# Kernel tuning notes

Measured on AMD Instinct MI355X. Metric: run time of the kernel, lower is better.

The kernel has to match this reference:

```python
import jax, jax.numpy as jnp
import numpy as np

B, D, L, N, M, K = 256, 512, 196, 1024, 512, 10000  # batch, context, num_ctx, hidden, embed, vocab


def setup_inputs() -> dict:
    key = jax.random.key(0)
    ks = jax.random.split(key, 20)
    r = lambda k, s: jax.random.normal(k, s, dtype=jnp.float32) * 0.02
    return {
        "a_i": jax.random.normal(ks[0], (B, D, L), dtype=jnp.float32),
        "inp": jax.random.normal(ks[1], (B, 1, K), dtype=jnp.float32),
        "hn_prev": jax.random.normal(ks[2], (B, 1, N), dtype=jnp.float32),
        "cn_prev": jax.random.normal(ks[3], (B, 1, N), dtype=jnp.float32),
        "f_att_w": r(ks[4], (N + D,)),  # Linear(n+D -> 1), stored as a vector
        "f_att_b": r(ks[5], (1,)),
        "gate_w": r(ks[6], (N,)),       # Linear(n -> 1)
        "gate_b": r(ks[7], (1,)),
        "E_w": r(ks[8], (M, K)),        # torch Linear weight [out, in]
        "E_b": r(ks[9], (M,)),
        "W_ih": r(ks[10], (4 * N, D + N + M)),  # LSTM input->hidden (i,f,g,o)
        "W_hh": r(ks[11], (4 * N, N)),
        "b_ih": r(ks[12], (4 * N,)),
        "b_hh": r(ks[13], (4 * N,)),
        "Lh_w": r(ks[14], (M, N)),
        "Lh_b": r(ks[15], (M,)),
        "Lz_w": r(ks[16], (M, D)),
        "Lz_b": r(ks[17], (M,)),
        "Lo_w": r(ks[18], (K, M)),
        "Lo_b": r(ks[19], (K,)),
    }


def reference(a_i, inp, hn_prev, cn_prev,
              f_att_w, f_att_b, gate_w, gate_b,
              E_w, E_b, W_ih, W_hh, b_ih, b_hh,
              Lh_w, Lh_b, Lz_w, Lz_b, Lo_w, Lo_b):
    h = hn_prev[:, 0]  # [B, N]
    c = cn_prev[:, 0]  # [B, N]
    # --- additive attention: the 196-iteration torch loop batched into one einsum ---
    # cat((a_i[:,:,i], h)) @ f_att_w splits into the a-part and h-part of the weight.
    w_a, w_h = f_att_w[:D], f_att_w[D:]
    e = jnp.einsum('bdl,d->bl', a_i, w_a) + (h @ w_h)[:, None] + f_att_b  # [B, L]
    alpha = jax.nn.softmax(e, axis=1)                                     # [B, L]
    beta = jax.nn.sigmoid(h @ gate_w + gate_b)                            # [B]
    z = beta[:, None] * jnp.einsum('bl,bdl->bd', alpha, a_i)              # [B, D]
    # --- word embedding ---
    w_emb = inp[:, 0] @ E_w.T + E_b                                       # [B, M]
    # --- single-step LSTM (PyTorch gate order i, f, g, o) ---
    x = jnp.concatenate([w_emb, h, z], axis=1)                            # [B, M+N+D]
    gates = x @ W_ih.T + b_ih + h @ W_hh.T + b_hh                         # [B, 4N]
    i_g, f_g, g_g, o_g = jnp.split(gates, 4, axis=1)
    cn = jax.nn.sigmoid(f_g) * c + jax.nn.sigmoid(i_g) * jnp.tanh(g_g)
    hn = jax.nn.sigmoid(o_g) * jnp.tanh(cn)
    # --- output projection ---
    deep_out = w_emb + (hn @ Lh_w.T + Lh_b) + (z @ Lz_w.T + Lz_b)         # [B, M]
    p_yt = deep_out @ Lo_w.T + Lo_b                                       # [B, K]
    return (p_yt[:, None, :], hn[:, None, :], cn[:, None, :], alpha[:, None, :])
```

## Files before the change

kernel.cpp:

```cpp
#include <hip/hip_runtime.h>
#include <hip/hip_bf16.h>
#include <math.h>

#define BB 256
#define DD 512
#define LL 196
#define NN 1024
#define MM 512
#define KK 10000

#define OUT_PY 0
#define OUT_HN ((size_t)2560000)
#define OUT_CN ((size_t)2822144)
#define OUT_AL ((size_t)3084288)

typedef __attribute__((ext_vector_type(8))) short short8v;
typedef __attribute__((ext_vector_type(4))) float f32x4;

__device__ __forceinline__ unsigned short f2bf(float f) {
    unsigned int u = __builtin_bit_cast(unsigned int, f);
    u += 0x7fffu + ((u >> 16) & 1u);
    return (unsigned short)(u >> 16);
}

__device__ __forceinline__ short8v stage8(const float* __restrict__ p, bool ok,
                                          int kbase, int Ktot) {
    short8v v;
    if (ok && (kbase + 7 < Ktot)) {
        const float4 x = *(const float4*)(p + kbase);
        const float4 y = *(const float4*)(p + kbase + 4);
        v[0] = (short)f2bf(x.x); v[1] = (short)f2bf(x.y);
        v[2] = (short)f2bf(x.z); v[3] = (short)f2bf(x.w);
        v[4] = (short)f2bf(y.x); v[5] = (short)f2bf(y.y);
        v[6] = (short)f2bf(y.z); v[7] = (short)f2bf(y.w);
    } else {
#pragma unroll
        for (int i = 0; i < 8; ++i) {
            const int k = kbase + i;
            const float f = (ok && k < Ktot) ? p[k] : 0.f;
            v[i] = (short)f2bf(f);
        }
    }
    return v;
}

__global__ __launch_bounds__(256) void att_e_partial(
    const float* __restrict__ a_i, const float* __restrict__ f_att_w,
    float* __restrict__ pe)
{
    const int b = blockIdx.x, ch = blockIdx.y;
    const int l = threadIdx.x;
    if (l >= LL) return;
    const float* ap = a_i + ((size_t)b * DD + ch * 64) * LL + l;
    const float* wp = f_att_w + ch * 64;
    float s = 0.f;
#pragma unroll 16
    for (int d = 0; d < 64; ++d) s += ap[(size_t)d * LL] * wp[d];
    pe[((size_t)b * 8 + ch) * LL + l] = s;
}

__global__ __launch_bounds__(256) void att_softmax(
    const float* __restrict__ pe, const float* __restrict__ h,
    const float* __restrict__ f_att_w, const float* __restrict__ f_att_b,
    const float* __restrict__ gate_w, const float* __restrict__ gate_b,
    float* __restrict__ alpha_out, float* __restrict__ beta)
{
    const int b = blockIdx.x;
    const int t = threadIdx.x;
    __shared__ float red[256];
    __shared__ float red2[256];

    const float4 h4 = *(const float4*)(h + (size_t)b * NN + t * 4);
    const float4 w4 = *(const float4*)(f_att_w + DD + t * 4);
    const float4 g4 = *(const float4*)(gate_w + t * 4);
    float hd = h4.x * w4.x + h4.y * w4.y + h4.z * w4.z + h4.w * w4.w;
    float gd = h4.x * g4.x + h4.y * g4.y + h4.z * g4.z + h4.w * g4.w;
    red[t] = hd; red2[t] = gd;
    __syncthreads();
    for (int s = 128; s > 0; s >>= 1) {
        if (t < s) { red[t] += red[t + s]; red2[t] += red2[t + s]; }
        __syncthreads();
    }
    const float hdot = red[0];
    const float gdot = red2[0];
    __syncthreads();

    float e = -3.4e38f;
    if (t < LL) {
        const float* p = pe + (size_t)b * 8 * LL + t;
        e = hdot + f_att_b[0];
#pragma unroll
        for (int ch = 0; ch < 8; ++ch) e += p[ch * LL];
    }
    red[t] = e;
    __syncthreads();
    for (int s = 128; s > 0; s >>= 1) {
        if (t < s) red[t] = fmaxf(red[t], red[t + s]);
        __syncthreads();
    }
    const float mx = red[0];
    __syncthreads();
    const float ex = (t < LL) ? expf(e - mx) : 0.f;
    red[t] = ex;
    __syncthreads();
    for (int s = 128; s > 0; s >>= 1) {
        if (t < s) red[t] += red[t + s];
        __syncthreads();
    }
    const float inv = 1.f / red[0];
    if (t < LL) alpha_out[(size_t)b * LL + t] = ex * inv;
    if (t == 0) beta[b] = 1.f / (1.f + expf(-(gdot + gate_b[0])));
}

__global__ __launch_bounds__(256) void att_z(
    const float* __restrict__ a_i, const float* __restrict__ alpha,
    const float* __restrict__ beta, float* __restrict__ z)
{
    const int b = blockIdx.x;
    const int wave = threadIdx.x >> 6, lane = threadIdx.x & 63;
    const int d = blockIdx.y * 4 + wave;
    const float* ap = a_i + ((size_t)b * DD + d) * LL;
    const float* alp = alpha + (size_t)b * LL;
    float s = 0.f;
#pragma unroll
    for (int i = 0; i < 4; ++i) {
        const int l = lane + i * 64;
        if (l < LL) s += ap[l] * alp[l];
    }
#pragma unroll
    for (int off = 32; off > 0; off >>= 1) s += __shfl_down(s, off, 64);
    if (lane == 0) z[(size_t)b * DD + d] = beta[b] * s;
}

__global__ __launch_bounds__(256) void gemm_tn_dual(
    const float* __restrict__ A1, int lda1, const float* __restrict__ B1, int ldb1,
    int kt1n, int K1,
    const float* __restrict__ A2, int lda2, const float* __restrict__ B2, int ldb2,
    int kt2n, int K2,
    float* __restrict__ C, int ldc, int Ncols, int ktPerSplit,
    const float* __restrict__ bias)
{
    __shared__ __align__(16) short As[2][64][72];
    __shared__ __align__(16) short Bs[2][64][72];
    const int t = threadIdx.x;
    const int row0 = blockIdx.x * 64;
    const int col0 = blockIdx.y * 64;
    const int ktTot = kt1n + kt2n;
    const int kt0 = blockIdx.z * ktPerSplit;
    const int nk = min(ktTot, kt0 + ktPerSplit) - kt0;

    const int sr = t >> 2;
    const int sk = (t & 3) << 4;
    const int bc = col0 + sr;
    const bool bok = (bc < Ncols);
    const float* aP1 = A1 + (size_t)(row0 + sr) * lda1;
    const float* bP1 = B1 + (size_t)(bok ? bc : 0) * ldb1;
    const float* aP2 = A2 ? (A2 + (size_t)(row0 + sr) * lda2) : aP1;
    const float* bP2 = A2 ? (B2 + (size_t)(bok ? bc : 0) * ldb2) : bP1;

    const int l = t & 63, w = t >> 6;
    const int wrow = (w >> 1) * 32, wcol = (w & 1) * 32;
    const int lr = l & 15, g = l >> 4, g8 = g * 8;

    f32x4 acc[2][2] = {};

    short8v sa0, sa1, sb0, sb1;
    {
        const int ktg = kt0;
        const float* aR; const float* bR; int kk, Kt;
        if (ktg < kt1n) { aR = aP1; bR = bP1; kk = (ktg << 6) + sk; Kt = K1; }
        else            { aR = aP2; bR = bP2; kk = ((ktg - kt1n) << 6) + sk; Kt = K2; }
        sa0 = stage8(aR, true, kk, Kt);  sa1 = stage8(aR, true, kk + 8, Kt);
        sb0 = stage8(bR, bok,  kk, Kt);  sb1 = stage8(bR, bok,  kk + 8, Kt);
    }
    *(short8v*)&As[0][sr][sk] = sa0; *(short8v*)&As[0][sr][sk + 8] = sa1;
    *(short8v*)&Bs[0][sr][sk] = sb0; *(short8v*)&Bs[0][sr][sk + 8] = sb1;
    __syncthreads();

    int cur = 0;
    for (int kt = 0; kt < nk; ++kt) {
        const bool more = (kt + 1 < nk);
        if (more) {
            const int ktg = kt0 + kt + 1;
            const float* aR; const float* bR; int kk, Kt;
            if (ktg < kt1n) { aR = aP1; bR = bP1; kk = (ktg << 6) + sk; Kt = K1; }
            else            { aR = aP2; bR = bP2; kk = ((ktg - kt1n) << 6) + sk; Kt = K2; }
            sa0 = stage8(aR, true, kk, Kt);  sa1 = stage8(aR, true, kk + 8, Kt);
            sb0 = stage8(bR, bok,  kk, Kt);  sb1 = stage8(bR, bok,  kk + 8, Kt);
        }
#pragma unroll
        for (int ks = 0; ks < 2; ++ks) {
            const int ko = ks * 32 + g8;
            short8v a0 = *(const short8v*)&As[cur][wrow + lr][ko];
            short8v a1 = *(const short8v*)&As[cur][wrow + 16 + lr][ko];
            short8v b0 = *(const short8v*)&Bs[cur][wcol + lr][ko];
            short8v b1 = *(const short8v*)&Bs[cur][wcol + 16 + lr][ko];
            acc[0][0] = __builtin_amdgcn_mfma_f32_16x16x32_bf16(a0, b0, acc[0][0], 0, 0, 0);
            acc[0][1] = __builtin_amdgcn_mfma_f32_16x16x32_bf16(a0, b1, acc[0][1], 0, 0, 0);
            acc[1][0] = __builtin_amdgcn_mfma_f32_16x16x32_bf16(a1, b0, acc[1][0], 0, 0, 0);
            acc[1][1] = __builtin_amdgcn_mfma_f32_16x16x32_bf16(a1, b1, acc[1][1], 0, 0, 0);
        }
        if (more) {
            *(short8v*)&As[cur ^ 1][sr][sk] = sa0;
            *(short8v*)&As[cur ^ 1][sr][sk + 8] = sa1;
            *(short8v*)&Bs[cur ^ 1][sr][sk] = sb0;
            *(short8v*)&Bs[cur ^ 1][sr][sk + 8] = sb1;
        }
        __syncthreads();
        cur ^= 1;
    }

    float* Cp = C + (size_t)blockIdx.z * ((size_t)gridDim.x * 64) * ldc;
#pragma unroll
    for (int m = 0; m < 2; ++m)
#pragma unroll
        for (int n = 0; n < 2; ++n)
#pragma unroll
            for (int j = 0; j < 4; ++j) {
                const int r = row0 + wrow + m * 16 + g * 4 + j;
                const int c = col0 + wcol + n * 16 + lr;
                if (c < Ncols) {
                    float v = acc[m][n][j];
                    if (bias) v += bias[c];
                    Cp[(size_t)r * ldc + c] = v;
                }
            }
}

__global__ __launch_bounds__(256) void build_x(
    const float* __restrict__ embp, int nEmb, const float* __restrict__ E_b,
    const float* __restrict__ h, const float* __restrict__ z,
    float* __restrict__ x)
{
    const int idx = blockIdx.x * 256 + threadIdx.x;
    const int b = idx >> 11, j = idx & 2047;
    float v;
    if (j < 512) {
        v = E_b[j];
        for (int s = 0; s < nEmb; ++s) v += embp[(size_t)s * BB * 512 + (size_t)b * 512 + j];
    } else if (j < 1536) {
        v = h[(size_t)b * NN + (j - 512)];
    } else {
        v = z[(size_t)b * DD + (j - 1536)];
    }
    x[idx] = v;
}

__global__ __launch_bounds__(256) void lstm_cell(
    const float* __restrict__ gatesp, int nG,
    const float* __restrict__ b_ih, const float* __restrict__ b_hh,
    const float* __restrict__ c_prev, float* __restrict__ hn, float* __restrict__ cn)
{
    const int idx = blockIdx.x * 256 + threadIdx.x;
    const int b = idx >> 10, n = idx & 1023;
    float g[4];
#pragma unroll
    for (int gi = 0; gi < 4; ++gi) {
        const int col = gi * 1024 + n;
        const size_t o = (size_t)b * 4096 + col;
        float v = b_ih[col] + b_hh[col];
        for (int s = 0; s < nG; ++s) v += gatesp[(size_t)s * BB * 4096 + o];
        g[gi] = v;
    }
    const float si = 1.f / (1.f + expf(-g[0]));
    const float sf = 1.f / (1.f + expf(-g[1]));
    const float so = 1.f / (1.f + expf(-g[3]));
    const float tg = tanhf(g[2]);
    const float c = c_prev[idx];
    const float cnv = sf * c + si * tg;
    const float hnv = so * tanhf(cnv);
    cn[idx] = cnv;
    hn[idx] = hnv;
}

__global__ __launch_bounds__(256) void build_deep(
    const float* __restrict__ x, const float* __restrict__ dp, int nD,
    const float* __restrict__ Lh_b, const float* __restrict__ Lz_b,
    float* __restrict__ deep)
{
    const int idx = blockIdx.x * 256 + threadIdx.x;
    const int b = idx >> 9, j = idx & 511;
    float v = x[(size_t)b * 2048 + j] + Lh_b[j] + Lz_b[j];
    for (int s = 0; s < nD; ++s) v += dp[(size_t)s * BB * 512 + idx];
    deep[idx] = v;
}

extern "C" void kernel_launch(void* const* d_in, const int* in_sizes, int n_in,
                              void* d_out, int out_size, void* d_ws, size_t ws_size,
                              hipStream_t stream)
{
    const float* a_i     = (const float*)d_in[0];
    const float* inp     = (const float*)d_in[1];
    const float* hn_prev = (const float*)d_in[2];
    const float* cn_prev = (const float*)d_in[3];
    const float* f_att_w = (const float*)d_in[4];
    const float* f_att_b = (const float*)d_in[5];
    const float* gate_w  = (const float*)d_in[6];
    const float* gate_b  = (const float*)d_in[7];
    const float* E_w     = (const float*)d_in[8];
    const float* E_b     = (const float*)d_in[9];
    const float* W_ih    = (const float*)d_in[10];
    const float* W_hh    = (const float*)d_in[11];
    const float* b_ih    = (const float*)d_in[12];
    const float* b_hh    = (const float*)d_in[13];
    const float* Lh_w    = (const float*)d_in[14];
    const float* Lh_b    = (const float*)d_in[15];
    const float* Lz_w    = (const float*)d_in[16];
    const float* Lz_b    = (const float*)d_in[17];
    const float* Lo_w    = (const float*)d_in[18];
    const float* Lo_b    = (const float*)d_in[19];

    float* out = (float*)d_out;
    float* ws  = (float*)d_ws;

    const size_t off_pe   = 0;
    const size_t off_beta = 401408;
    const size_t off_z    = 401664;
    const size_t off_x    = 532736;
    const size_t off_deep = 1057024;
    const size_t small_end = 1188096;

    const size_t avail = ws_size / sizeof(float);
    const bool big = (avail >= small_end + (size_t)4194304);
    const int embS = big ? 16 : 4;
    const int gS   = big ? 4 : 2;
    const int dS   = big ? 12 : 4;
    const size_t off_r1 = small_end;

    float* EMBP   = ws + off_r1;
    float* GATESP = ws + off_r1;
    float* DP     = ws + off_r1;

    att_e_partial<<<dim3(BB, 8), 256, 0, stream>>>(a_i, f_att_w, ws + off_pe);
    att_softmax<<<BB, 256, 0, stream>>>(ws + off_pe, hn_prev, f_att_w, f_att_b,
                                        gate_w, gate_b, out + OUT_AL, ws + off_beta);
    att_z<<<dim3(BB, DD / 4), 256, 0, stream>>>(a_i, out + OUT_AL, ws + off_beta,
                                                ws + off_z);

    gemm_tn_dual<<<dim3(4, 8, embS), 256, 0, stream>>>(
        inp, KK, E_w, KK, 157, KK,
        nullptr, 0, nullptr, 0, 0, 0,
        EMBP, MM, MM, (157 + embS - 1) / embS, nullptr);

    build_x<<<BB * 2048 / 256, 256, 0, stream>>>(EMBP, embS, E_b, hn_prev,
                                                 ws + off_z, ws + off_x);

    gemm_tn_dual<<<dim3(4, 64, gS), 256, 0, stream>>>(
        ws + off_x, 2048, W_ih, 2048, 32, 2048,
        hn_prev, NN, W_hh, NN, 16, NN,
        GATESP, 4096, 4096, 48 / gS, nullptr);

    lstm_cell<<<BB * NN / 256, 256, 0, stream>>>(GATESP, gS, b_ih, b_hh,
                                                 cn_prev, out + OUT_HN, out + OUT_CN);

    gemm_tn_dual<<<dim3(4, 8, dS), 256, 0, stream>>>(
        out + OUT_HN, NN, Lh_w, NN, 16, NN,
        ws + off_z, DD, Lz_w, DD, 8, DD,
        DP, MM, MM, 24 / dS, nullptr);

    build_deep<<<BB * MM / 256, 256, 0, stream>>>(ws + off_x, DP, dS,
                                                  Lh_b, Lz_b, ws + off_deep);

    gemm_tn_dual<<<dim3(4, 157, 1), 256, 0, stream>>>(
        ws + off_deep, MM, Lo_w, MM, 8, MM,
        nullptr, 0, nullptr, 0, 0, 0,
        out + OUT_PY, KK, KK, 8, Lo_b);
}
```

Before: 168.1 us.

## Fuse independent stages into shared launches and split LSTM gate GEMM by dependency

Restructures the pipeline so independent work shares one launch: the attention-score partials run alongside the embedding GEMM, the softmax runs alongside the embedding split-K reduction, and the attention context reduction runs alongside the h-dependent part of the gate GEMM. The gate GEMM is split so the W_hh and h-slice of W_ih are computed before z and the embedding are ready, removing the concatenated x buffer and its build kernel. Split-K counts and workspace offsets are now fixed, which drops the small-workspace fallback and assumes a large workspace. It also switches bf16 conversion to the library intrinsic and gives the reduction loops constant trip counts.

```diff
diff --git a/kernel.cpp b/kernel.cpp
--- a/kernel.cpp
+++ b/kernel.cpp
@@ -14,13 +14,21 @@
 #define OUT_CN ((size_t)2822144)
 #define OUT_AL ((size_t)3084288)
 
+#define OFF_PE    ((size_t)0)
+#define OFF_BETA  ((size_t)401408)
+#define OFF_Z     ((size_t)401664)
+#define OFF_EMB   ((size_t)532736)
+#define OFF_DEEP  ((size_t)663808)
+#define OFF_EMBP  ((size_t)794880)
+#define OFF_GATESP ((size_t)2892032)
+#define OFF_DP    ((size_t)9183488)
+
 typedef __attribute__((ext_vector_type(8))) short short8v;
 typedef __attribute__((ext_vector_type(4))) float f32x4;
 
-__device__ __forceinline__ unsigned short f2bf(float f) {
-    unsigned int u = __builtin_bit_cast(unsigned int, f);
-    u += 0x7fffu + ((u >> 16) & 1u);
-    return (unsigned short)(u >> 16);
+__device__ __forceinline__ short bfs(float f) {
+    __hip_bfloat16 h = __float2bfloat16(f);
+    return *reinterpret_cast<short*>(&h);
 }
 
 __device__ __forceinline__ short8v stage8(const float* __restrict__ p, bool ok,
@@ -29,134 +37,42 @@
     if (ok && (kbase + 7 < Ktot)) {
         const float4 x = *(const float4*)(p + kbase);
         const float4 y = *(const float4*)(p + kbase + 4);
-        v[0] = (short)f2bf(x.x); v[1] = (short)f2bf(x.y);
-        v[2] = (short)f2bf(x.z); v[3] = (short)f2bf(x.w);
-        v[4] = (short)f2bf(y.x); v[5] = (short)f2bf(y.y);
-        v[6] = (short)f2bf(y.z); v[7] = (short)f2bf(y.w);
+        v[0] = bfs(x.x); v[1] = bfs(x.y); v[2] = bfs(x.z); v[3] = bfs(x.w);
+        v[4] = bfs(y.x); v[5] = bfs(y.y); v[6] = bfs(y.z); v[7] = bfs(y.w);
     } else {
 #pragma unroll
         for (int i = 0; i < 8; ++i) {
             const int k = kbase + i;
-            const float f = (ok && k < Ktot) ? p[k] : 0.f;
-            v[i] = (short)f2bf(f);
+            v[i] = bfs((ok && k < Ktot) ? p[k] : 0.f);
         }
     }
     return v;
 }
 
-__global__ __launch_bounds__(256) void att_e_partial(
-    const float* __restrict__ a_i, const float* __restrict__ f_att_w,
-    float* __restrict__ pe)
-{
-    const int b = blockIdx.x, ch = blockIdx.y;
-    const int l = threadIdx.x;
-    if (l >= LL) return;
-    const float* ap = a_i + ((size_t)b * DD + ch * 64) * LL + l;
-    const float* wp = f_att_w + ch * 64;
-    float s = 0.f;
-#pragma unroll 16
-    for (int d = 0; d < 64; ++d) s += ap[(size_t)d * LL] * wp[d];
-    pe[((size_t)b * 8 + ch) * LL + l] = s;
-}
-
-__global__ __launch_bounds__(256) void att_softmax(
-    const float* __restrict__ pe, const float* __restrict__ h,
-    const float* __restrict__ f_att_w, const float* __restrict__ f_att_b,
-    const float* __restrict__ gate_w, const float* __restrict__ gate_b,
-    float* __restrict__ alpha_out, float* __restrict__ beta)
-{
-    const int b = blockIdx.x;
+struct GSrc { const float* A; int lda; const float* B; int ldb; int ktn; int K; };
+
+__device__ __forceinline__ void gemm_body(
+    const int bx, const int by, const int bz, const int rowBlocks,
+    const GSrc s1, const GSrc s2,
+    float* __restrict__ C, const int ldc, const int Ncols,
+    const int ktPerSplit, const float* __restrict__ bias,
+    short (*As)[64][72], short (*Bs)[64][72])
+{
     const int t = threadIdx.x;
-    __shared__ float red[256];
-    __shared__ float red2[256];
-
-    const float4 h4 = *(const float4*)(h + (size_t)b * NN + t * 4);
-    const float4 w4 = *(const float4*)(f_att_w + DD + t * 4);
-    const float4 g4 = *(const float4*)(gate_w + t * 4);
-    float hd = h4.x * w4.x + h4.y * w4.y + h4.z * w4.z + h4.w * w4.w;
-    float gd = h4.x * g4.x + h4.y * g4.y + h4.z * g4.z + h4.w * g4.w;
-    red[t] = hd; red2[t] = gd;
-    __syncthreads();
-    for (int s = 128; s > 0; s >>= 1) {
-        if (t < s) { red[t] += red[t + s]; red2[t] += red2[t + s]; }
-        __syncthreads();
-    }
-    const float hdot = red[0];
-    const float gdot = red2[0];
-    __syncthreads();
-
-    float e = -3.4e38f;
-    if (t < LL) {
-        const float* p = pe + (size_t)b * 8 * LL + t;
-        e = hdot + f_att_b[0];
-#pragma unroll
-        for (int ch = 0; ch < 8; ++ch) e += p[ch * LL];
-    }
-    red[t] = e;
-    __syncthreads();
-    for (int s = 128; s > 0; s >>= 1) {
-        if (t < s) red[t] = fmaxf(red[t], red[t + s]);
-        __syncthreads();
-    }
-    const float mx = red[0];
-    __syncthreads();
-    const float ex = (t < LL) ? expf(e - mx) : 0.f;
-    red[t] = ex;
-    __syncthreads();
-    for (int s = 128; s > 0; s >>= 1) {
-        if (t < s) red[t] += red[t + s];
-        __syncthreads();
-    }
-    const float inv = 1.f / red[0];
-    if (t < LL) alpha_out[(size_t)b * LL + t] = ex * inv;
-    if (t == 0) beta[b] = 1.f / (1.f + expf(-(gdot + gate_b[0])));
-}
-
-__global__ __launch_bounds__(256) void att_z(
-    const float* __restrict__ a_i, const float* __restrict__ alpha,
-    const float* __restrict__ beta, float* __restrict__ z)
-{
-    const int b = blockIdx.x;
-    const int wave = threadIdx.x >> 6, lane = threadIdx.x & 63;
-    const int d = blockIdx.y * 4 + wave;
-    const float* ap = a_i + ((size_t)b * DD + d) * LL;
-    const float* alp = alpha + (size_t)b * LL;
-    float s = 0.f;
-#pragma unroll
-    for (int i = 0; i < 4; ++i) {
-        const int l = lane + i * 64;
-        if (l < LL) s += ap[l] * alp[l];
-    }
-#pragma unroll
-    for (int off = 32; off > 0; off >>= 1) s += __shfl_down(s, off, 64);
-    if (lane == 0) z[(size_t)b * DD + d] = beta[b] * s;
-}
-
-__global__ __launch_bounds__(256) void gemm_tn_dual(
-    const float* __restrict__ A1, int lda1, const float* __restrict__ B1, int ldb1,
-    int kt1n, int K1,
-    const float* __restrict__ A2, int lda2, const float* __restrict__ B2, int ldb2,
-    int kt2n, int K2,
-    float* __restrict__ C, int ldc, int Ncols, int ktPerSplit,
-    const float* __restrict__ bias)
-{
-    __shared__ __align__(16) short As[2][64][72];
-    __shared__ __align__(16) short Bs[2][64][72];
-    const int t = threadIdx.x;
-    const int row0 = blockIdx.x * 64;
-    const int col0 = blockIdx.y * 64;
-    const int ktTot = kt1n + kt2n;
-    const int kt0 = blockIdx.z * ktPerSplit;
+    const int row0 = bx * 64;
+    const int col0 = by * 64;
+    const int ktTot = s1.ktn + s2.ktn;
+    const int kt0 = bz * ktPerSplit;
     const int nk = min(ktTot, kt0 + ktPerSplit) - kt0;
 
     const int sr = t >> 2;
     const int sk = (t & 3) << 4;
     const int bc = col0 + sr;
     const bool bok = (bc < Ncols);
-    const float* aP1 = A1 + (size_t)(row0 + sr) * lda1;
-    const float* bP1 = B1 + (size_t)(bok ? bc : 0) * ldb1;
-    const float* aP2 = A2 ? (A2 + (size_t)(row0 + sr) * lda2) : aP1;
-    const float* bP2 = A2 ? (B2 + (size_t)(bok ? bc : 0) * ldb2) : bP1;
+    const float* aP1 = s1.A + (size_t)(row0 + sr) * s1.lda;
+    const float* bP1 = s1.B + (size_t)(bok ? bc : 0) * s1.ldb;
+    const float* aP2 = s2.A ? (s2.A + (size_t)(row0 + sr) * s2.lda) : aP1;
+    const float* bP2 = s2.A ? (s2.B + (size_t)(bok ? bc : 0) * s2.ldb) : bP1;
 
     const int l = t & 63, w = t >> 6;
     const int wrow = (w >> 1) * 32, wcol = (w & 1) * 32;
@@ -168,8 +84,8 @@
     {
         const int ktg = kt0;
         const float* aR; const float* bR; int kk, Kt;
-        if (ktg < kt1n) { aR = aP1; bR = bP1; kk = (ktg << 6) + sk; Kt = K1; }
-        else            { aR = aP2; bR = bP2; kk = ((ktg - kt1n) << 6) + sk; Kt = K2; }
+        if (ktg < s1.ktn) { aR = aP1; bR = bP1; kk = (ktg << 6) + sk; Kt = s1.K; }
+        else              { aR = aP2; bR = bP2; kk = ((ktg - s1.ktn) << 6) + sk; Kt = s2.K; }
         sa0 = stage8(aR, true, kk, Kt);  sa1 = stage8(aR, true, kk + 8, Kt);
         sb0 = stage8(bR, bok,  kk, Kt);  sb1 = stage8(bR, bok,  kk + 8, Kt);
     }
@@ -183,8 +99,8 @@
         if (more) {
             const int ktg = kt0 + kt + 1;
             const float* aR; const float* bR; int kk, Kt;
-            if (ktg < kt1n) { aR = aP1; bR = bP1; kk = (ktg << 6) + sk; Kt = K1; }
-            else            { aR = aP2; bR = bP2; kk = ((ktg - kt1n) << 6) + sk; Kt = K2; }
+            if (ktg < s1.ktn) { aR = aP1; bR = bP1; kk = (ktg << 6) + sk; Kt = s1.K; }
+            else              { aR = aP2; bR = bP2; kk = ((ktg - s1.ktn) << 6) + sk; Kt = s2.K; }
             sa0 = stage8(aR, true, kk, Kt);  sa1 = stage8(aR, true, kk + 8, Kt);
             sb0 = stage8(bR, bok,  kk, Kt);  sb1 = stage8(bR, bok,  kk + 8, Kt);
         }
@@ -210,7 +126,7 @@
         cur ^= 1;
     }
 
-    float* Cp = C + (size_t)blockIdx.z * ((size_t)gridDim.x * 64) * ldc;
+    float* Cp = C + (size_t)bz * ((size_t)rowBlocks * 64) * ldc;
 #pragma unroll
     for (int m = 0; m < 2; ++m)
 #pragma unroll
@@ -227,27 +143,157 @@
             }
 }
 
-__global__ __launch_bounds__(256) void build_x(
-    const float* __restrict__ embp, int nEmb, const float* __restrict__ E_b,
-    const float* __restrict__ h, const float* __restrict__ z,
-    float* __restrict__ x)
-{
-    const int idx = blockIdx.x * 256 + threadIdx.x;
-    const int b = idx >> 11, j = idx & 2047;
-    float v;
-    if (j < 512) {
-        v = E_b[j];
-        for (int s = 0; s < nEmb; ++s) v += embp[(size_t)s * BB * 512 + (size_t)b * 512 + j];
-    } else if (j < 1536) {
-        v = h[(size_t)b * NN + (j - 512)];
+__global__ __launch_bounds__(256) void p1_atte_emb(
+    const float* __restrict__ a_i, const float* __restrict__ f_att_w,
+    float* __restrict__ pe,
+    const float* __restrict__ inp, const float* __restrict__ E_w,
+    float* __restrict__ embp)
+{
+    __shared__ __align__(16) short As[2][64][72];
+    __shared__ __align__(16) short Bs[2][64][72];
+    const int bid = blockIdx.x;
+    if (bid < 2048) {
+        const int b = bid >> 3, ch = bid & 7;
+        const int l = threadIdx.x;
+        if (l >= LL) return;
+        const float* ap = a_i + ((size_t)b * DD + ch * 64) * LL + l;
+        const float* wp = f_att_w + ch * 64;
+        float s = 0.f;
+#pragma unroll 16
+        for (int d = 0; d < 64; ++d) s += ap[(size_t)d * LL] * wp[d];
+        pe[((size_t)b * 8 + ch) * LL + l] = s;
     } else {
-        v = z[(size_t)b * DD + (j - 1536)];
-    }
-    x[idx] = v;
-}
-
-__global__ __launch_bounds__(256) void lstm_cell(
-    const float* __restrict__ gatesp, int nG,
+        const int i = bid - 2048;
+        GSrc s1 = {inp, KK, E_w, KK, 157, KK};
+        GSrc s2 = {nullptr, 0, nullptr, 0, 0, 0};
+        gemm_body(i & 3, (i >> 2) & 7, i >> 5, 4, s1, s2,
+                  embp, MM, MM, 10, nullptr, As, Bs);
+    }
+}
+
+__global__ __launch_bounds__(256) void p2_softmax_embred(
+    const float* __restrict__ pe, const float* __restrict__ h,
+    const float* __restrict__ f_att_w, const float* __restrict__ f_att_b,
+    const float* __restrict__ gate_w, const float* __restrict__ gate_b,
+    float* __restrict__ alpha_out, float* __restrict__ beta,
+    const float* __restrict__ embp, const float* __restrict__ E_b,
+    float* __restrict__ emb)
+{
+    const int bid = blockIdx.x;
+    const int t = threadIdx.x;
+    if (bid < 256) {
+        const int b = bid;
+        __shared__ float red[256];
+        __shared__ float red2[256];
+        const float4 h4 = *(const float4*)(h + (size_t)b * NN + t * 4);
+        const float4 w4 = *(const float4*)(f_att_w + DD + t * 4);
+        const float4 g4 = *(const float4*)(gate_w + t * 4);
+        float hd = h4.x * w4.x + h4.y * w4.y + h4.z * w4.z + h4.w * w4.w;
+        float gd = h4.x * g4.x + h4.y * g4.y + h4.z * g4.z + h4.w * g4.w;
+        red[t] = hd; red2[t] = gd;
+        __syncthreads();
+        for (int s = 128; s > 0; s >>= 1) {
+            if (t < s) { red[t] += red[t + s]; red2[t] += red2[t + s]; }
+            __syncthreads();
+        }
+        const float hdot = red[0];
+        const float gdot = red2[0];
+        __syncthreads();
+        float e = -3.4e38f;
+        if (t < LL) {
+            const float* p = pe + (size_t)b * 8 * LL + t;
+            e = hdot + f_att_b[0];
+#pragma unroll
+            for (int ch = 0; ch < 8; ++ch) e += p[ch * LL];
+        }
+        red[t] = e;
+        __syncthreads();
+        for (int s = 128; s > 0; s >>= 1) {
+            if (t < s) red[t] = fmaxf(red[t], red[t + s]);
+            __syncthreads();
+        }
+        const float mx = red[0];
+        __syncthreads();
+        const float ex = (t < LL) ? expf(e - mx) : 0.f;
+        red[t] = ex;
+        __syncthreads();
+        for (int s = 128; s > 0; s >>= 1) {
+            if (t < s) red[t] += red[t + s];
+            __syncthreads();
+        }
+        const float inv = 1.f / red[0];
+        if (t < LL) alpha_out[(size_t)b * LL + t] = ex * inv;
+        if (t == 0) beta[b] = 1.f / (1.f + expf(-(gdot + gate_b[0])));
+    } else {
+        const int idx = (bid - 256) * 256 + t;
+        const int j = idx & 511;
+        float v = E_b[j];
+#pragma unroll
+        for (int s = 0; s < 16; ++s) v += embp[(size_t)s * (BB * 512) + idx];
+        emb[idx] = v;
+    }
+}
+
+__global__ __launch_bounds__(256) void p3_attz_gatesh(
+    const float* __restrict__ a_i, const float* __restrict__ alpha,
+    const float* __restrict__ beta, float* __restrict__ z,
+    const float* __restrict__ h, const float* __restrict__ W_ih,
+    const float* __restrict__ W_hh, float* __restrict__ gatesp)
+{
+    __shared__ __align__(16) short As[2][64][72];
+    __shared__ __align__(16) short Bs[2][64][72];
+    const int bid = blockIdx.x;
+    if (bid < 8192) {
+        const int b = bid >> 5, chunk = bid & 31;
+        const int wave = threadIdx.x >> 6, lane = threadIdx.x & 63;
+        const float* alp = alpha + (size_t)b * LL;
+#pragma unroll
+        for (int i = 0; i < 4; ++i) {
+            const int d = chunk * 16 + wave * 4 + i;
+            const float* ap = a_i + ((size_t)b * DD + d) * LL;
+            float s = 0.f;
+#pragma unroll
+            for (int q = 0; q < 4; ++q) {
+                const int lidx = lane + q * 64;
+                if (lidx < LL) s += ap[lidx] * alp[lidx];
+            }
+#pragma unroll
+            for (int off = 32; off > 0; off >>= 1) s += __shfl_down(s, off, 64);
+            if (lane == 0) z[(size_t)b * DD + d] = beta[b] * s;
+        }
+    } else {
+        const int i = bid - 8192;
+        GSrc s1 = {h, NN, W_ih + 512, 2048, 16, NN};
+        GSrc s2 = {h, NN, W_hh, NN, 16, NN};
+        gemm_body(i & 3, (i >> 2) & 63, i >> 8, 4, s1, s2,
+                  gatesp, 4096, 4096, 8, nullptr, As, Bs);
+    }
+}
+
+__global__ __launch_bounds__(256) void p4_gatesez_lz(
+    const float* __restrict__ emb, const float* __restrict__ z,
+    const float* __restrict__ W_ih, float* __restrict__ gatesp_hi,
+    const float* __restrict__ Lz_w, float* __restrict__ dp)
+{
+    __shared__ __align__(16) short As[2][64][72];
+    __shared__ __align__(16) short Bs[2][64][72];
+    const int bid = blockIdx.x;
+    if (bid < 512) {
+        GSrc s1 = {emb, MM, W_ih, 2048, 8, MM};
+        GSrc s2 = {z, DD, W_ih + 1536, 2048, 8, DD};
+        gemm_body(bid & 3, (bid >> 2) & 63, bid >> 8, 4, s1, s2,
+                  gatesp_hi, 4096, 4096, 8, nullptr, As, Bs);
+    } else {
+        const int i = bid - 512;
+        GSrc s1 = {z, DD, Lz_w, DD, 8, DD};
+        GSrc s2 = {nullptr, 0, nullptr, 0, 0, 0};
+        gemm_body(i & 3, (i >> 2) & 7, i >> 5, 4, s1, s2,
+                  dp, MM, MM, 1, nullptr, As, Bs);
+    }
+}
+
+__global__ __launch_bounds__(256) void p5_lstm(
+    const float* __restrict__ gatesp,
     const float* __restrict__ b_ih, const float* __restrict__ b_hh,
     const float* __restrict__ c_prev, float* __restrict__ hn, float* __restrict__ cn)
 {
@@ -259,7 +305,8 @@
         const int col = gi * 1024 + n;
         const size_t o = (size_t)b * 4096 + col;
         float v = b_ih[col] + b_hh[col];
-        for (int s = 0; s < nG; ++s) v += gatesp[(size_t)s * BB * 4096 + o];
+#pragma unroll
+        for (int s = 0; s < 6; ++s) v += gatesp[(size_t)s * (BB * 4096) + o];
         g[gi] = v;
     }
     const float si = 1.f / (1.f + expf(-g[0]));
@@ -273,16 +320,43 @@
     hn[idx] = hnv;
 }
 
-__global__ __launch_bounds__(256) void build_deep(
-    const float* __restrict__ x, const float* __restrict__ dp, int nD,
+__global__ __launch_bounds__(256) void p6_lh(
+    const float* __restrict__ hn, const float* __restrict__ Lh_w,
+    float* __restrict__ dp_hi)
+{
+    __shared__ __align__(16) short As[2][64][72];
+    __shared__ __align__(16) short Bs[2][64][72];
+    const int bid = blockIdx.x;
+    GSrc s1 = {hn, NN, Lh_w, NN, 16, NN};
+    GSrc s2 = {nullptr, 0, nullptr, 0, 0, 0};
+    gemm_body(bid & 3, (bid >> 2) & 7, bid >> 5, 4, s1, s2,
+              dp_hi, MM, MM, 1, nullptr, As, Bs);
+}
+
+__global__ __launch_bounds__(256) void p7_deep(
+    const float* __restrict__ emb, const float* __restrict__ dp,
     const float* __restrict__ Lh_b, const float* __restrict__ Lz_b,
     float* __restrict__ deep)
 {
     const int idx = blockIdx.x * 256 + threadIdx.x;
-    const int b = idx >> 9, j = idx & 511;
-    float v = x[(size_t)b * 2048 + j] + Lh_b[j] + Lz_b[j];
-    for (int s = 0; s < nD; ++s) v += dp[(size_t)s * BB * 512 + idx];
+    const int j = idx & 511;
+    float v = emb[idx] + Lh_b[j] + Lz_b[j];
+#pragma unroll
+    for (int s = 0; s < 24; ++s) v += dp[(size_t)s * (BB * 512) + idx];
     deep[idx] = v;
+}
+
+__global__ __launch_bounds__(256) void p8_pyt(
+    const float* __restrict__ deep, const float* __restrict__ Lo_w,
+    const float* __restrict__ Lo_b, float* __restrict__ out)
+{
+    __shared__ __align__(16) short As[2][64][72];
+    __shared__ __align__(16) short Bs[2][64][72];
+    const int bid = blockIdx.x;
+    GSrc s1 = {deep, MM, Lo_w, MM, 8, MM};
+    GSrc s2 = {nullptr, 0, nullptr, 0, 0, 0};
+    gemm_body(bid & 3, bid >> 2, 0, 4, s1, s2,
+              out, KK, KK, 8, Lo_b, As, Bs);
 }
 
 extern "C" void kernel_launch(void* const* d_in, const int* in_sizes, int n_in,
@@ -313,56 +387,35 @@
     float* out = (float*)d_out;
     float* ws  = (float*)d_ws;
 
-    const size_t off_pe   = 0;
-    const size_t off_beta = 401408;
-    const size_t off_z    = 401664;
-    const size_t off_x    = 532736;
-    const size_t off_deep = 1057024;
-    const size_t small_end = 1188096;
-
-    const size_t avail = ws_size / sizeof(float);
-    const bool big = (avail >= small_end + (size_t)4194304);
-    const int embS = big ? 16 : 4;
-    const int gS   = big ? 4 : 2;
-    const int dS   = big ? 12 : 4;
-    const size_t off_r1 = small_end;
-
-    float* EMBP   = ws + off_r1;
-    float* GATESP = ws + off_r1;
-    float* DP     = ws + off_r1;
-
-    att_e_partial<<<dim3(BB, 8), 256, 0, stream>>>(a_i, f_att_w, ws + off_pe);
-    att_softmax<<<BB, 256, 0, stream>>>(ws + off_pe, hn_prev, f_att_w, f_att_b,
-                                        gate_w, gate_b, out + OUT_AL, ws + off_beta);
-    att_z<<<dim3(BB, DD / 4), 256, 0, stream>>>(a_i, out + OUT_AL, ws + off_beta,
-                                                ws + off_z);
-
-    gemm_tn_dual<<<dim3(4, 8, embS), 256, 0, stream>>>(
-        inp, KK, E_w, KK, 157, KK,
-        nullptr, 0, nullptr, 0, 0, 0,
-        EMBP, MM, MM, (157 + embS - 1) / embS, nullptr);
-
-    build_x<<<BB * 2048 / 256, 256, 0, stream>>>(EMBP, embS, E_b, hn_prev,
-                                                 ws + off_z, ws + off_x);
-
-    gemm_tn_dual<<<dim3(4, 64, gS), 256, 0, stream>>>(
-        ws + off_x, 2048, W_ih, 2048, 32, 2048,
-        hn_prev, NN, W_hh, NN, 16, NN,
-        GATESP, 4096, 4096, 48 / gS, nullptr);
-
-    lstm_cell<<<BB * NN / 256, 256, 0, stream>>>(GATESP, gS, b_ih, b_hh,
-                                                 cn_prev, out + OUT_HN, out + OUT_CN);
-
-    gemm_tn_dual<<<dim3(4, 8, dS), 256, 0, stream>>>(
-        out + OUT_HN, NN, Lh_w, NN, 16, NN,
-        ws + off_z, DD, Lz_w, DD, 8, DD,
-        DP, MM, MM, 24 / dS, nullptr);
-
-    build_deep<<<BB * MM / 256, 256, 0, stream>>>(ws + off_x, DP, dS,
-                                                  Lh_b, Lz_b, ws + off_deep);
-
-    gemm_tn_dual<<<dim3(4, 157, 1), 256, 0, stream>>>(
-        ws + off_deep, MM, Lo_w, MM, 8, MM,
-        nullptr, 0, nullptr, 0, 0, 0,
-        out + OUT_PY, KK, KK, 8, Lo_b);
-}
+    float* PE     = ws + OFF_PE;
+    float* BETA   = ws + OFF_BETA;
+    float* Z      = ws + OFF_Z;
+    float* EMB    = ws + OFF_EMB;
+    float* DEEP   = ws + OFF_DEEP;
+    float* EMBP   = ws + OFF_EMBP;
+    float* GATESP = ws + OFF_GATESP;
+    float* DP     = ws + OFF_DP;
+
+    p1_atte_emb<<<2560, 256, 0, stream>>>(a_i, f_att_w, PE, inp, E_w, EMBP);
+
+    p2_softmax_embred<<<768, 256, 0, stream>>>(PE, hn_prev, f_att_w, f_att_b,
+                                               gate_w, gate_b, out + OUT_AL, BETA,
+                                               EMBP, E_b, EMB);
+
+    p3_attz_gatesh<<<9216, 256, 0, stream>>>(a_i, out + OUT_AL, BETA, Z,
+                                             hn_prev, W_ih, W_hh, GATESP);
+
+    p4_gatesez_lz<<<768, 256, 0, stream>>>(EMB, Z, W_ih,
+                                           GATESP + (size_t)4 * BB * 4096,
+                                           Lz_w, DP);
+
+    p5_lstm<<<1024, 256, 0, stream>>>(GATESP, b_ih, b_hh, cn_prev,
+                                      out + OUT_HN, out + OUT_CN);
+
+    p6_lh<<<512, 256, 0, stream>>>(out + OUT_HN, Lh_w,
+                                   DP + (size_t)8 * BB * 512);
+
+    p7_deep<<<512, 256, 0, stream>>>(EMB, DP, Lh_b, Lz_b, DEEP);
+
+    p8_pyt<<<628, 256, 0, stream>>>(DEEP, Lo_w, Lo_b, out + OUT_PY);
+}
```

Result: faster. 156.9 us (-6.7%).
